# Performance work log

Measured on AMD Instinct MI355X. Metric: run time of the kernel, lower is better.

Reference implementation:

```python
import jax, jax.numpy as jnp
import numpy as np
import math

B, N, DMODEL, H = 8, 1024, 256, 8
HEAD_DIM = DMODEL // H


def setup_inputs() -> dict:
    key = jax.random.key(0)
    ks = jax.random.split(key, 8)
    x = jax.random.normal(ks[0], (B, N, DMODEL), dtype=jnp.float32)
    # symmetric-ish nonnegative pairwise distances
    adj = jax.random.uniform(ks[1], (B, N, N), dtype=jnp.float32) * 10.0
    mask = jax.random.uniform(ks[2], (B, N)) < 0.9  # bool, mostly valid nodes
    W_qkv = jax.random.normal(ks[3], (DMODEL, 3 * DMODEL), dtype=jnp.float32) / math.sqrt(DMODEL)
    b_qkv = jax.random.normal(ks[4], (3 * DMODEL,), dtype=jnp.float32) * 0.01
    shifts = jnp.arange(1.0, H + 1.0, dtype=jnp.float32)  # initial_shifts
    widths = jnp.ones((H,), dtype=jnp.float32)            # initial_widths
    # self_loop_W = 1/head_dim + U(0,1), non-trainable
    self_loop_w = 1.0 / HEAD_DIM + jax.random.uniform(ks[5], (H,), dtype=jnp.float32)
    return {"x": x, "adj": adj, "mask": mask, "W_qkv": W_qkv, "b_qkv": b_qkv,
            "shifts": shifts, "widths": widths, "self_loop_w": self_loop_w}


def reference(x, adj, mask, W_qkv, b_qkv, shifts, widths, self_loop_w):
    b, n, _ = x.shape
    h = shifts.shape[0]
    d = W_qkv.shape[1] // (3 * h)
    qkv = (x @ W_qkv + b_qkv).reshape(b, n, 3, h, d)
    qkv = jnp.transpose(qkv, (2, 0, 3, 1, 4))  # [3, B, H, N, D]
    Q, K, V = qkv[0], qkv[1], qkv[2]
    scores = jnp.einsum('bhnd,bhmd->bhnm', Q, K) / jnp.sqrt(jnp.float32(d))
    # Gaussian moire focus on adjacency distances, per head
    sh = shifts.reshape(1, h, 1, 1)
    w = jnp.maximum(widths, 0.5).reshape(1, h, 1, 1)
    moire = jnp.exp(-((adj[:, None, :, :] - sh) ** 2) / w)
    adjusted = scores + jnp.log(jnp.maximum(moire, 1e-6))
    eye = jnp.eye(n, dtype=adjusted.dtype)  # [N, N]
    adjusted = adjusted + eye * self_loop_w.reshape(1, h, 1, 1)
    mask2d = (mask[:, :, None] & mask[:, None, :])[:, None, :, :]  # [B,1,N,N]
    adjusted = jnp.where(mask2d, adjusted, jnp.float32(-1000000.0))
    attn = jax.nn.softmax(adjusted, axis=-1)
    out = jnp.einsum('bhnm,bhmd->bhnd', attn, V)
    return jnp.transpose(out, (0, 2, 1, 3)).reshape(b, n, h * d)
```

## Files before the change

### kernel.cpp

```cpp
#include <hip/hip_runtime.h>

#define BB 8
#define NN 1024
#define DM 256
#define HH 8
#define HD 32
#define TC 768

typedef __bf16 bf16x8 __attribute__((ext_vector_type(8)));
typedef __bf16 bf16x4 __attribute__((ext_vector_type(4)));
typedef float  f32x4  __attribute__((ext_vector_type(4)));
typedef int    i32x4  __attribute__((ext_vector_type(4)));
typedef unsigned int u32;

__global__ __launch_bounds__(256) void precast(
    const float* __restrict__ x, const float* __restrict__ W,
    __bf16* __restrict__ xb, __bf16* __restrict__ Wt)
{
  const int tid = threadIdx.x;
  const int bid = blockIdx.x;
  if (bid < 48) {
    __shared__ __bf16 T[64][65];
    const int ct = bid % 12, kt = bid / 12;
    const int c0 = ct * 64, k0 = kt * 64;
    #pragma unroll
    for (int i = 0; i < 16; ++i) {
      int e = tid + i * 256, kk = e >> 6, cc = e & 63;
      T[cc][kk] = (__bf16)W[(size_t)(k0 + kk) * TC + c0 + cc];
    }
    __syncthreads();
    #pragma unroll
    for (int i = 0; i < 16; ++i) {
      int e = tid + i * 256, cc = e >> 6, kk = e & 63;
      Wt[(size_t)(c0 + cc) * DM + k0 + kk] = T[cc][kk];
    }
  } else {
    const size_t e = (size_t)(bid - 48) * 256 + tid;
    const float4 v = ((const float4*)x)[e];
    bf16x4 o;
    o[0] = (__bf16)v.x; o[1] = (__bf16)v.y;
    o[2] = (__bf16)v.z; o[3] = (__bf16)v.w;
    ((bf16x4*)xb)[e] = o;
  }
}

__global__ __launch_bounds__(256, 3) void qkv_gemm(
    const __bf16* __restrict__ xb, const __bf16* __restrict__ Wt,
    const float* __restrict__ bias, __bf16* __restrict__ Qb,
    __bf16* __restrict__ Kb, __bf16* __restrict__ Vt)
{
  __shared__ __align__(16) char LDSU[49152];
  __bf16* As0 = (__bf16*)LDSU;
  __bf16* Bs0 = (__bf16*)(LDSU + 16384);
  __bf16* As1 = (__bf16*)(LDSU + 24576);
  __bf16* Bs1 = (__bf16*)(LDSU + 40960);

  const int tid  = threadIdx.x;
  const int w    = tid >> 6, lane = tid & 63;
  const int n16  = lane & 15, quad = lane >> 4;
  const int m0   = blockIdx.y * 128, c0 = blockIdx.x * 64;
  const int bb   = m0 >> 10, n0 = m0 & 1023;

  const int stRow = w*8 + (lane >> 3);
  const int stG   = (lane & 7) ^ (lane >> 3);
  const __bf16* gA = &xb[(size_t)(m0 + stRow)*DM + stG*8];
  const __bf16* gB = &Wt[(size_t)(c0 + stRow)*DM + stG*8];

#define QKV_STAGE(Adst, Bdst, K0) do {                                        \
    _Pragma("unroll")                                                         \
    for (int i_ = 0; i_ < 4; ++i_) {                                          \
      const __bf16* gp_ = gA + (size_t)(i_*32)*DM + (K0);                     \
      __bf16* lp_ = (Adst) + (i_*32 + w*8)*64;                                \
      __builtin_amdgcn_global_load_lds(                                       \
          (const __attribute__((address_space(1))) u32*)gp_,                  \
          (__attribute__((address_space(3))) u32*)lp_, 16, 0, 0);             \
    }                                                                         \
    _Pragma("unroll")                                                         \
    for (int i_ = 0; i_ < 2; ++i_) {                                          \
      const __bf16* gp_ = gB + (size_t)(i_*32)*DM + (K0);                     \
      __bf16* lp_ = (Bdst) + (i_*32 + w*8)*64;                                \
      __builtin_amdgcn_global_load_lds(                                       \
          (const __attribute__((address_space(1))) u32*)gp_,                  \
          (__attribute__((address_space(3))) u32*)lp_, 16, 0, 0);             \
    }                                                                         \
  } while (0)

  f32x4 acc[2][4] = {};

  QKV_STAGE(As0, Bs0, 0);
  __syncthreads();

  #pragma unroll
  for (int kk = 0; kk < 4; ++kk) {
    __bf16* Ac = (kk & 1) ? As1 : As0;
    __bf16* Bc = (kk & 1) ? Bs1 : Bs0;
    if (kk == 0)      QKV_STAGE(As1, Bs1, 64);
    else if (kk == 1) QKV_STAGE(As0, Bs0, 128);
    else if (kk == 2) QKV_STAGE(As1, Bs1, 192);
    #pragma unroll
    for (int ks = 0; ks < 2; ++ks) {
      const int ch = ((ks*4 + quad) ^ (n16 & 7)) * 8;
      bf16x8 af0 = *(const bf16x8*)&Ac[(w*32 + n16)*64 + ch];
      bf16x8 af1 = *(const bf16x8*)&Ac[(w*32 + 16 + n16)*64 + ch];
      #pragma unroll
      for (int cb = 0; cb < 4; ++cb) {
        bf16x8 bfb = *(const bf16x8*)&Bc[(cb*16 + n16)*64 + ch];
        acc[0][cb] = __builtin_amdgcn_mfma_f32_16x16x32_bf16(af0, bfb, acc[0][cb], 0, 0, 0);
        acc[1][cb] = __builtin_amdgcn_mfma_f32_16x16x32_bf16(af1, bfb, acc[1][cb], 0, 0, 0);
      }
    }
    __syncthreads();
  }

  float bv[4];
  #pragma unroll
  for (int cb = 0; cb < 4; ++cb) bv[cb] = bias[c0 + cb*16 + n16];

  if (c0 < 512) {
    __bf16* Ct = (__bf16*)LDSU;
    #pragma unroll
    for (int cb = 0; cb < 4; ++cb)
      #pragma unroll
      for (int mb = 0; mb < 2; ++mb)
        #pragma unroll
        for (int r = 0; r < 4; ++r)
          Ct[(w*32 + mb*16 + quad*4 + r)*72 + cb*16 + n16] =
              (__bf16)(acc[mb][cb][r] + bv[cb]);
    __syncthreads();
    const int chunk = tid & 3, hh = (tid >> 2) & 1, rbase = tid >> 3;
    const int c_head = c0 + hh*32;
    const int h = (c_head >> 5) & 7;
    __bf16* base = (c_head >> 8) ? Kb : Qb;
    #pragma unroll
    for (int it = 0; it < 4; ++it) {
      int rl = rbase + it*32;
      bf16x8 v = *(const bf16x8*)&Ct[rl*72 + hh*32 + chunk*8];
      *(bf16x8*)&base[((size_t)((bb*HH + h)*NN + n0 + rl))*HD + chunk*8] = v;
    }
  } else {
    __bf16* CtT = (__bf16*)LDSU;
    #pragma unroll
    for (int cb = 0; cb < 4; ++cb)
      #pragma unroll
      for (int mb = 0; mb < 2; ++mb) {
        bf16x4 t;
        #pragma unroll
        for (int r = 0; r < 4; ++r) t[r] = (__bf16)(acc[mb][cb][r] + bv[cb]);
        *(bf16x4*)&CtT[(cb*16 + n16)*136 + w*32 + mb*16 + quad*4] = t;
      }
    __syncthreads();
    const int col = tid >> 2, sg = tid & 3;
    const int c = c0 + col;
    const int h = (c >> 5) & 7, dd = c & 31;
    __bf16* dst = &Vt[((size_t)((bb*HH + h)*HD + dd))*NN + n0 + sg*32];
    const __bf16* srcp = &CtT[col*136 + sg*32];
    #pragma unroll
    for (int q2 = 0; q2 < 4; ++q2)
      *(bf16x8*)&dst[q2*8] = *(const bf16x8*)&srcp[q2*8];
  }
}

__global__ __launch_bounds__(256, 4) void attn_kernel(
    const __bf16* __restrict__ Q, const __bf16* __restrict__ K,
    const __bf16* __restrict__ Vt, const float* __restrict__ adj,
    const int* __restrict__ mask, const float* __restrict__ shifts,
    const float* __restrict__ widths, const float* __restrict__ slw,
    float* __restrict__ out)
{
  __shared__ __align__(16) __bf16 Ks[2][64][40];
  __shared__ __align__(16) __bf16 Vts[2][32][72];

  const int tid  = threadIdx.x;
  const int w    = tid >> 6, lane = tid & 63;
  const int n16  = lane & 15, quad = lane >> 4;
  const int bh   = blockIdx.x >> 4, qt = blockIdx.x & 15;
  const int b    = bh >> 3, h = bh & 7;
  const int q0   = qt * 64;

  const float L2E   = 1.4426950408889634f;
  const float sh    = shifts[h];
  const float ninvw = -L2E / fmaxf(widths[h], 0.5f);
  const float slv   = slw[h] * L2E;
  const float scl   = 0.17677669529663687f * L2E;
  const float MASKV = -28.0f;
  const float c1 = -2.0f * sh * ninvw;
  const float c2 = sh * sh * ninvw;

  const int srow = tid >> 2, sseg = tid & 3;
  const int phiRow = (srow & 35) + (((srow >> 2) & 1) << 4) + (((srow >> 3) & 3) << 2);
  const int vd   = tid >> 3, vsg  = tid & 7;

  const __bf16* Kg = K + (size_t)bh*NN*HD;
  const __bf16* Vg = Vt + (size_t)bh*HD*NN;

  const bf16x8 qf =
      *(const bf16x8*)&Q[((size_t)bh*NN + q0 + w*16 + n16)*HD + quad*8];

  {
    *(bf16x8*)&Ks[0][phiRow][sseg*8] = *(const bf16x8*)&Kg[srow*HD + sseg*8];
    *(bf16x8*)&Vts[0][vd][vsg*8]     = *(const bf16x8*)&Vg[(size_t)vd*NN + vsg*8];
  }

  const bool mqv = mask[b*NN + q0 + w*16 + n16] != 0;

  const float* aqp = adj + ((size_t)(b*NN + q0 + w*16 + n16))*NN + 8*quad;
  const int*   mjp = mask + b*NN + 8*quad;

  f32x4 av[2][2][2];
  #pragma unroll
  for (int a = 0; a < 2; ++a)
    #pragma unroll
    for (int b2 = 0; b2 < 2; ++b2)
      av[0][a][b2] = *(const f32x4*)&aqp[32*a + 4*b2];

  const int dloc8 = w*16 + n16 - 8*quad;

  const f32x4 zero = {0.f, 0.f, 0.f, 0.f};
  f32x4 o0 = zero, o1 = zero, lacc = zero;
  bf16x8 onesb;
  #pragma unroll
  for (int i = 0; i < 8; ++i) onesb[i] = (__bf16)1.0f;

  __syncthreads();

  #pragma unroll 2
  for (int jtl = 0; jtl < 16; ++jtl) {
    const int cur = jtl & 1, nxt = cur ^ 1;
    const int j0  = jtl * 64;

    bf16x8 kn, vn;
    if (jtl < 15) {
      kn = *(const bf16x8*)&Kg[(j0 + 64 + srow)*HD + sseg*8];
      vn = *(const bf16x8*)&Vg[(size_t)vd*NN + j0 + 64 + vsg*8];
      #pragma unroll
      for (int a = 0; a < 2; ++a)
        #pragma unroll
        for (int b2 = 0; b2 < 2; ++b2)
          av[nxt][a][b2] = *(const f32x4*)&aqp[j0 + 64 + 32*a + 4*b2];
    }

    i32x4 mj[2][2];
    #pragma unroll
    for (int a = 0; a < 2; ++a)
      #pragma unroll
      for (int b2 = 0; b2 < 2; ++b2)
        mj[a][b2] = *(const i32x4*)&mjp[j0 + 32*a + 4*b2];

    f32x4 s[4];
    #pragma unroll
    for (int c = 0; c < 4; ++c) {
      bf16x8 kf = *(const bf16x8*)&Ks[cur][c*16 + n16][quad*8];
      s[c] = __builtin_amdgcn_mfma_f32_16x16x32_bf16(kf, qf, zero, 0, 0, 0);
    }

    const bool diagtile = (jtl == qt);
    bf16x8 pa0, pa1;
    #pragma unroll
    for (int a = 0; a < 2; ++a)
      #pragma unroll
      for (int b2 = 0; b2 < 2; ++b2) {
        const int c = 2*a + b2;
        #pragma unroll
        for (int r = 0; r < 4; ++r) {
          float ad  = av[cur][a][b2][r];
          float mo  = fmaf(ad, fmaf(ad, ninvw, c1), c2);
          float val = fmaf(s[c][r], scl, mo);
          if (diagtile && (32*a + 4*b2 + r) == dloc8) val += slv;
          bool ok = mqv && (mj[a][b2][r] != 0);
          val = ok ? val : MASKV;
          float p = __builtin_amdgcn_exp2f(val);
          if (a == 0) pa0[4*b2 + r] = (__bf16)p;
          else        pa1[4*b2 + r] = (__bf16)p;
        }
      }

    bf16x8 b00 = *(const bf16x8*)&Vts[cur][n16][quad*8];
    bf16x8 b01 = *(const bf16x8*)&Vts[cur][n16][32 + quad*8];
    bf16x8 b10 = *(const bf16x8*)&Vts[cur][16 + n16][quad*8];
    bf16x8 b11 = *(const bf16x8*)&Vts[cur][16 + n16][32 + quad*8];
    o0   = __builtin_amdgcn_mfma_f32_16x16x32_bf16(pa0, b00, o0, 0, 0, 0);
    o0   = __builtin_amdgcn_mfma_f32_16x16x32_bf16(pa1, b01, o0, 0, 0, 0);
    o1   = __builtin_amdgcn_mfma_f32_16x16x32_bf16(pa0, b10, o1, 0, 0, 0);
    o1   = __builtin_amdgcn_mfma_f32_16x16x32_bf16(pa1, b11, o1, 0, 0, 0);
    lacc = __builtin_amdgcn_mfma_f32_16x16x32_bf16(pa0, onesb, lacc, 0, 0, 0);
    lacc = __builtin_amdgcn_mfma_f32_16x16x32_bf16(pa1, onesb, lacc, 0, 0, 0);

    if (jtl < 15) {
      *(bf16x8*)&Ks[nxt][phiRow][sseg*8] = kn;
      *(bf16x8*)&Vts[nxt][vd][vsg*8]     = vn;
    }
    __syncthreads();
  }

  #pragma unroll
  for (int r = 0; r < 4; ++r) {
    const float invl = 1.0f / lacc[r];
    const int n = q0 + w*16 + quad*4 + r;
    float* og = out + ((size_t)(b*NN + n))*DM + h*HD;
    og[n16]      = o0[r] * invl;
    og[16 + n16] = o1[r] * invl;
  }
}

extern "C" void kernel_launch(void* const* d_in, const int* in_sizes, int n_in,
                              void* d_out, int out_size, void* d_ws, size_t ws_size,
                              hipStream_t stream) {
  const float* x      = (const float*)d_in[0];
  const float* adj    = (const float*)d_in[1];
  const int*   mask   = (const int*)d_in[2];
  const float* W      = (const float*)d_in[3];
  const float* bias   = (const float*)d_in[4];
  const float* shifts = (const float*)d_in[5];
  const float* widths = (const float*)d_in[6];
  const float* slwp   = (const float*)d_in[7];
  float* out = (float*)d_out;

  const size_t BHND = (size_t)BB*HH*NN*HD;
  const size_t WTN  = (size_t)TC*DM;
  __bf16* xbuf = (__bf16*)d_ws;
  __bf16* Wt   = xbuf + BHND;
  __bf16* Qb   = Wt + WTN;
  __bf16* Kb   = Qb + BHND;
  __bf16* Vt   = Kb + BHND;

  precast<<<dim3(48 + (int)(BHND/4/256)), 256, 0, stream>>>(x, W, xbuf, Wt);
  qkv_gemm<<<dim3(TC/64, (BB*NN)/128), 256, 0, stream>>>(xbuf, Wt, bias, Qb, Kb, Vt);
  attn_kernel<<<dim3(BB*HH*16), 256, 0, stream>>>(Qb, Kb, Vt, adj, mask,
                                                  shifts, widths, slwp, out);
}
```

Baseline: 147.9 us.

## Remap key-to-lane layout and interleave exp computation with PV MFMAs

Changes which key columns each lane owns. K rows are now stored unpermuted, and V^T is permuted in LDS with split bf16x4 loads, so each lane reads adj and mask as four contiguous 16-column chunks instead of the earlier 32/4 interleave. The probability computation is split into two halves, and the first half's PV and row-sum MFMAs are issued before the second half's exp work, so matrix and vector work can overlap. The V loads become two narrower 8-byte global accesses per thread, which may cost some global-load efficiency.

```diff
diff --git a/kernel.cpp b/kernel.cpp
--- a/kernel.cpp
+++ b/kernel.cpp
@@ -187,8 +187,9 @@
   const float c2 = sh * sh * ninvw;
 
   const int srow = tid >> 2, sseg = tid & 3;
-  const int phiRow = (srow & 35) + (((srow >> 2) & 1) << 4) + (((srow >> 3) & 3) << 2);
   const int vd   = tid >> 3, vsg  = tid & 7;
+  const int vA   = (vsg & 4) << 3;
+  const int vq   = vsg & 3;
 
   const __bf16* Kg = K + (size_t)bh*NN*HD;
   const __bf16* Vg = Vt + (size_t)bh*HD*NN;
@@ -197,23 +198,21 @@
       *(const bf16x8*)&Q[((size_t)bh*NN + q0 + w*16 + n16)*HD + quad*8];
 
   {
-    *(bf16x8*)&Ks[0][phiRow][sseg*8] = *(const bf16x8*)&Kg[srow*HD + sseg*8];
-    *(bf16x8*)&Vts[0][vd][vsg*8]     = *(const bf16x8*)&Vg[(size_t)vd*NN + vsg*8];
+    *(bf16x8*)&Ks[0][srow][sseg*8] = *(const bf16x8*)&Kg[srow*HD + sseg*8];
+    *(bf16x4*)&Vts[0][vd][vsg*8]     = *(const bf16x4*)&Vg[(size_t)vd*NN + vA + 4*vq];
+    *(bf16x4*)&Vts[0][vd][vsg*8 + 4] = *(const bf16x4*)&Vg[(size_t)vd*NN + vA + 16 + 4*vq];
   }
 
   const bool mqv = mask[b*NN + q0 + w*16 + n16] != 0;
 
-  const float* aqp = adj + ((size_t)(b*NN + q0 + w*16 + n16))*NN + 8*quad;
-  const int*   mjp = mask + b*NN + 8*quad;
-
-  f32x4 av[2][2][2];
-  #pragma unroll
-  for (int a = 0; a < 2; ++a)
-    #pragma unroll
-    for (int b2 = 0; b2 < 2; ++b2)
-      av[0][a][b2] = *(const f32x4*)&aqp[32*a + 4*b2];
-
-  const int dloc8 = w*16 + n16 - 8*quad;
+  const float* aqp = adj + ((size_t)(b*NN + q0 + w*16 + n16))*NN + 4*quad;
+  const int*   mjp = mask + b*NN + 4*quad;
+
+  f32x4 av[2][4];
+  #pragma unroll
+  for (int c = 0; c < 4; ++c) av[0][c] = *(const f32x4*)&aqp[16*c];
+
+  const int dloc = w*16 + n16 - 4*quad;
 
   const f32x4 zero = {0.f, 0.f, 0.f, 0.f};
   f32x4 o0 = zero, o1 = zero, lacc = zero;
@@ -228,23 +227,19 @@
     const int cur = jtl & 1, nxt = cur ^ 1;
     const int j0  = jtl * 64;
 
-    bf16x8 kn, vn;
+    bf16x8 kn; bf16x4 vn0, vn1;
     if (jtl < 15) {
-      kn = *(const bf16x8*)&Kg[(j0 + 64 + srow)*HD + sseg*8];
-      vn = *(const bf16x8*)&Vg[(size_t)vd*NN + j0 + 64 + vsg*8];
-      #pragma unroll
-      for (int a = 0; a < 2; ++a)
-        #pragma unroll
-        for (int b2 = 0; b2 < 2; ++b2)
-          av[nxt][a][b2] = *(const f32x4*)&aqp[j0 + 64 + 32*a + 4*b2];
-    }
-
-    i32x4 mj[2][2];
-    #pragma unroll
-    for (int a = 0; a < 2; ++a)
-      #pragma unroll
-      for (int b2 = 0; b2 < 2; ++b2)
-        mj[a][b2] = *(const i32x4*)&mjp[j0 + 32*a + 4*b2];
+      kn  = *(const bf16x8*)&Kg[(j0 + 64 + srow)*HD + sseg*8];
+      vn0 = *(const bf16x4*)&Vg[(size_t)vd*NN + j0 + 64 + vA + 4*vq];
+      vn1 = *(const bf16x4*)&Vg[(size_t)vd*NN + j0 + 64 + vA + 16 + 4*vq];
+      #pragma unroll
+      for (int c = 0; c < 4; ++c)
+        av[nxt][c] = *(const f32x4*)&aqp[j0 + 64 + 16*c];
+    }
+
+    i32x4 mj[4];
+    #pragma unroll
+    for (int c = 0; c < 4; ++c) mj[c] = *(const i32x4*)&mjp[j0 + 16*c];
 
     f32x4 s[4];
     #pragma unroll
@@ -252,42 +247,49 @@
       bf16x8 kf = *(const bf16x8*)&Ks[cur][c*16 + n16][quad*8];
       s[c] = __builtin_amdgcn_mfma_f32_16x16x32_bf16(kf, qf, zero, 0, 0, 0);
     }
-
-    const bool diagtile = (jtl == qt);
-    bf16x8 pa0, pa1;
-    #pragma unroll
-    for (int a = 0; a < 2; ++a)
-      #pragma unroll
-      for (int b2 = 0; b2 < 2; ++b2) {
-        const int c = 2*a + b2;
-        #pragma unroll
-        for (int r = 0; r < 4; ++r) {
-          float ad  = av[cur][a][b2][r];
-          float mo  = fmaf(ad, fmaf(ad, ninvw, c1), c2);
-          float val = fmaf(s[c][r], scl, mo);
-          if (diagtile && (32*a + 4*b2 + r) == dloc8) val += slv;
-          bool ok = mqv && (mj[a][b2][r] != 0);
-          val = ok ? val : MASKV;
-          float p = __builtin_amdgcn_exp2f(val);
-          if (a == 0) pa0[4*b2 + r] = (__bf16)p;
-          else        pa1[4*b2 + r] = (__bf16)p;
-        }
-      }
 
     bf16x8 b00 = *(const bf16x8*)&Vts[cur][n16][quad*8];
     bf16x8 b01 = *(const bf16x8*)&Vts[cur][n16][32 + quad*8];
     bf16x8 b10 = *(const bf16x8*)&Vts[cur][16 + n16][quad*8];
     bf16x8 b11 = *(const bf16x8*)&Vts[cur][16 + n16][32 + quad*8];
+
+    const bool diagtile = (jtl == qt);
+    bf16x8 pa0, pa1;
+    #pragma unroll
+    for (int c = 0; c < 2; ++c)
+      #pragma unroll
+      for (int r = 0; r < 4; ++r) {
+        float ad  = av[cur][c][r];
+        float mo  = fmaf(ad, fmaf(ad, ninvw, c1), c2);
+        float val = fmaf(s[c][r], scl, mo);
+        if (diagtile && (16*c + r == dloc)) val += slv;
+        bool ok = mqv && (mj[c][r] != 0);
+        val = ok ? val : MASKV;
+        pa0[c*4 + r] = (__bf16)__builtin_amdgcn_exp2f(val);
+      }
     o0   = __builtin_amdgcn_mfma_f32_16x16x32_bf16(pa0, b00, o0, 0, 0, 0);
+    o1   = __builtin_amdgcn_mfma_f32_16x16x32_bf16(pa0, b10, o1, 0, 0, 0);
+    lacc = __builtin_amdgcn_mfma_f32_16x16x32_bf16(pa0, onesb, lacc, 0, 0, 0);
+    #pragma unroll
+    for (int c = 2; c < 4; ++c)
+      #pragma unroll
+      for (int r = 0; r < 4; ++r) {
+        float ad  = av[cur][c][r];
+        float mo  = fmaf(ad, fmaf(ad, ninvw, c1), c2);
+        float val = fmaf(s[c][r], scl, mo);
+        if (diagtile && (16*c + r == dloc)) val += slv;
+        bool ok = mqv && (mj[c][r] != 0);
+        val = ok ? val : MASKV;
+        pa1[(c & 1)*4 + r] = (__bf16)__builtin_amdgcn_exp2f(val);
+      }
     o0   = __builtin_amdgcn_mfma_f32_16x16x32_bf16(pa1, b01, o0, 0, 0, 0);
-    o1   = __builtin_amdgcn_mfma_f32_16x16x32_bf16(pa0, b10, o1, 0, 0, 0);
     o1   = __builtin_amdgcn_mfma_f32_16x16x32_bf16(pa1, b11, o1, 0, 0, 0);
-    lacc = __builtin_amdgcn_mfma_f32_16x16x32_bf16(pa0, onesb, lacc, 0, 0, 0);
     lacc = __builtin_amdgcn_mfma_f32_16x16x32_bf16(pa1, onesb, lacc, 0, 0, 0);
 
     if (jtl < 15) {
-      *(bf16x8*)&Ks[nxt][phiRow][sseg*8] = kn;
-      *(bf16x8*)&Vts[nxt][vd][vsg*8]     = vn;
+      *(bf16x8*)&Ks[nxt][srow][sseg*8]     = kn;
+      *(bf16x4*)&Vts[nxt][vd][vsg*8]       = vn0;
+      *(bf16x4*)&Vts[nxt][vd][vsg*8 + 4]   = vn1;
     }
     __syncthreads();
   }
```

Measured after the change: 151.3 us. +2.3%, slower.

## Share adjacency tiles across heads by assigning one head per wave

Applied to the files above, without the earlier changes.

The attention kernel now gives each block 32 query rows and 4 heads, one head per wave. The fp32 adjacency tile is staged once in shared memory and read by all four heads, so each adj row is fetched from global memory twice rather than eight times. Each wave handles its own K/V tile in private LDS buffers and routes P through LDS to reach the MFMA A-layout. The cost is more LDS traffic and bank pressure, fewer blocks (512), lower occupancy (launch bounds 2), and a block-wide barrier each tile.

```diff
diff --git a/kernel.cpp b/kernel.cpp
--- a/kernel.cpp
+++ b/kernel.cpp
@@ -10,7 +10,6 @@
 typedef __bf16 bf16x8 __attribute__((ext_vector_type(8)));
 typedef __bf16 bf16x4 __attribute__((ext_vector_type(4)));
 typedef float  f32x4  __attribute__((ext_vector_type(4)));
-typedef int    i32x4  __attribute__((ext_vector_type(4)));
 typedef unsigned int u32;
 
 __global__ __launch_bounds__(256) void precast(
@@ -160,22 +159,27 @@
   }
 }
 
-__global__ __launch_bounds__(256, 4) void attn_kernel(
+__global__ __launch_bounds__(256, 2) void attn_kernel(
     const __bf16* __restrict__ Q, const __bf16* __restrict__ K,
     const __bf16* __restrict__ Vt, const float* __restrict__ adj,
     const int* __restrict__ mask, const float* __restrict__ shifts,
     const float* __restrict__ widths, const float* __restrict__ slw,
     float* __restrict__ out)
 {
-  __shared__ __align__(16) __bf16 Ks[2][64][40];
-  __shared__ __align__(16) __bf16 Vts[2][32][72];
+  __shared__ __align__(16) __bf16 Ks[4][64][40];
+  __shared__ __align__(16) __bf16 Vts[4][32][72];
+  __shared__ __align__(16) float  As[2][32][68];
+  __shared__ __align__(16) __bf16 Ps[4][16][72];
 
   const int tid  = threadIdx.x;
   const int w    = tid >> 6, lane = tid & 63;
   const int n16  = lane & 15, quad = lane >> 4;
-  const int bh   = blockIdx.x >> 4, qt = blockIdx.x & 15;
-  const int b    = bh >> 3, h = bh & 7;
-  const int q0   = qt * 64;
+  const int hg   = blockIdx.x & 1;
+  const int qt   = (blockIdx.x >> 1) & 31;
+  const int b    = blockIdx.x >> 6;
+  const int h    = hg*4 + w;
+  const int bh   = b*HH + h;
+  const int q0   = qt * 32;
 
   const float L2E   = 1.4426950408889634f;
   const float sh    = shifts[h];
@@ -186,120 +190,133 @@
   const float c1 = -2.0f * sh * ninvw;
   const float c2 = sh * sh * ninvw;
 
-  const int srow = tid >> 2, sseg = tid & 3;
-  const int phiRow = (srow & 35) + (((srow >> 2) & 1) << 4) + (((srow >> 3) & 3) << 2);
-  const int vd   = tid >> 3, vsg  = tid & 7;
-
   const __bf16* Kg = K + (size_t)bh*NN*HD;
   const __bf16* Vg = Vt + (size_t)bh*HD*NN;
 
-  const bf16x8 qf =
-      *(const bf16x8*)&Q[((size_t)bh*NN + q0 + w*16 + n16)*HD + quad*8];
+  const __bf16* kgp = Kg + (size_t)lane*HD;
+  const int vdr = lane >> 1, vc0 = (lane & 1)*32;
+  const __bf16* vgp = Vg + (size_t)vdr*NN + vc0;
+  const int arow = tid >> 3, ac = (tid & 7)*4;
+  const float* agp = adj + ((size_t)(b*NN + q0 + arow))*NN + ac;
+  const int* mjp = mask + b*NN + n16;
+
+  const bf16x8 qf0 = *(const bf16x8*)&Q[((size_t)bh*NN + q0 +      n16)*HD + quad*8];
+  const bf16x8 qf1 = *(const bf16x8*)&Q[((size_t)bh*NN + q0 + 16 + n16)*HD + quad*8];
+  int mq[2][4];
+  #pragma unroll
+  for (int g = 0; g < 2; ++g)
+    #pragma unroll
+    for (int r = 0; r < 4; ++r)
+      mq[g][r] = mask[b*NN + q0 + g*16 + quad*4 + r];
 
   {
-    *(bf16x8*)&Ks[0][phiRow][sseg*8] = *(const bf16x8*)&Kg[srow*HD + sseg*8];
-    *(bf16x8*)&Vts[0][vd][vsg*8]     = *(const bf16x8*)&Vg[(size_t)vd*NN + vsg*8];
-  }
-
-  const bool mqv = mask[b*NN + q0 + w*16 + n16] != 0;
-
-  const float* aqp = adj + ((size_t)(b*NN + q0 + w*16 + n16))*NN + 8*quad;
-  const int*   mjp = mask + b*NN + 8*quad;
-
-  f32x4 av[2][2][2];
-  #pragma unroll
-  for (int a = 0; a < 2; ++a)
-    #pragma unroll
-    for (int b2 = 0; b2 < 2; ++b2)
-      av[0][a][b2] = *(const f32x4*)&aqp[32*a + 4*b2];
-
-  const int dloc8 = w*16 + n16 - 8*quad;
+    bf16x8 k0[4], v0[4]; f32x4 aa, ab;
+    #pragma unroll
+    for (int c = 0; c < 4; ++c) k0[c] = *(const bf16x8*)&kgp[c*8];
+    #pragma unroll
+    for (int i = 0; i < 4; ++i) v0[i] = *(const bf16x8*)&vgp[i*8];
+    aa = *(const f32x4*)&agp[0]; ab = *(const f32x4*)&agp[32];
+    #pragma unroll
+    for (int c = 0; c < 4; ++c) *(bf16x8*)&Ks[w][lane][c*8] = k0[c];
+    #pragma unroll
+    for (int i = 0; i < 4; ++i) *(bf16x8*)&Vts[w][vdr][vc0 + i*8] = v0[i];
+    *(f32x4*)&As[0][arow][ac]      = aa;
+    *(f32x4*)&As[0][arow][32 + ac] = ab;
+  }
+  int mj[4];
+  #pragma unroll
+  for (int cb = 0; cb < 4; ++cb) mj[cb] = mjp[cb*16];
 
   const f32x4 zero = {0.f, 0.f, 0.f, 0.f};
-  f32x4 o0 = zero, o1 = zero, lacc = zero;
+  f32x4 o0[2] = {zero, zero}, o1[2] = {zero, zero}, lacc[2] = {zero, zero};
   bf16x8 onesb;
   #pragma unroll
   for (int i = 0; i < 8; ++i) onesb[i] = (__bf16)1.0f;
 
+  const int diagT = qt >> 1;
+  const int dbase = (qt & 1) * 32;
+
   __syncthreads();
 
-  #pragma unroll 2
   for (int jtl = 0; jtl < 16; ++jtl) {
-    const int cur = jtl & 1, nxt = cur ^ 1;
+    const int cur = jtl & 1;
     const int j0  = jtl * 64;
 
-    bf16x8 kn, vn;
+    bf16x8 kn[4], vn[4]; f32x4 an0, an1; int mjn[4];
     if (jtl < 15) {
-      kn = *(const bf16x8*)&Kg[(j0 + 64 + srow)*HD + sseg*8];
-      vn = *(const bf16x8*)&Vg[(size_t)vd*NN + j0 + 64 + vsg*8];
-      #pragma unroll
-      for (int a = 0; a < 2; ++a)
+      #pragma unroll
+      for (int c = 0; c < 4; ++c) kn[c] = *(const bf16x8*)&kgp[(size_t)(j0+64)*HD + c*8];
+      #pragma unroll
+      for (int i = 0; i < 4; ++i) vn[i] = *(const bf16x8*)&vgp[j0 + 64 + i*8];
+      an0 = *(const f32x4*)&agp[j0 + 64];
+      an1 = *(const f32x4*)&agp[j0 + 96];
+      #pragma unroll
+      for (int cb = 0; cb < 4; ++cb) mjn[cb] = mjp[j0 + 64 + cb*16];
+    }
+
+    bf16x8 b00 = *(const bf16x8*)&Vts[w][n16][quad*8];
+    bf16x8 b01 = *(const bf16x8*)&Vts[w][n16][32 + quad*8];
+    bf16x8 b10 = *(const bf16x8*)&Vts[w][16 + n16][quad*8];
+    bf16x8 b11 = *(const bf16x8*)&Vts[w][16 + n16][32 + quad*8];
+
+    const bool diagtile = (jtl == diagT);
+
+    #pragma unroll
+    for (int g = 0; g < 2; ++g) {
+      const bf16x8 qf = g ? qf1 : qf0;
+      f32x4 s[4];
+      #pragma unroll
+      for (int cb = 0; cb < 4; ++cb) {
+        bf16x8 kf = *(const bf16x8*)&Ks[w][cb*16 + n16][quad*8];
+        s[cb] = __builtin_amdgcn_mfma_f32_16x16x32_bf16(qf, kf, zero, 0, 0, 0);
+      }
+      const int dref = dbase + g*16 + quad*4;
+      #pragma unroll
+      for (int r = 0; r < 4; ++r) {
         #pragma unroll
-        for (int b2 = 0; b2 < 2; ++b2)
-          av[nxt][a][b2] = *(const f32x4*)&aqp[j0 + 64 + 32*a + 4*b2];
-    }
-
-    i32x4 mj[2][2];
-    #pragma unroll
-    for (int a = 0; a < 2; ++a)
-      #pragma unroll
-      for (int b2 = 0; b2 < 2; ++b2)
-        mj[a][b2] = *(const i32x4*)&mjp[j0 + 32*a + 4*b2];
-
-    f32x4 s[4];
-    #pragma unroll
-    for (int c = 0; c < 4; ++c) {
-      bf16x8 kf = *(const bf16x8*)&Ks[cur][c*16 + n16][quad*8];
-      s[c] = __builtin_amdgcn_mfma_f32_16x16x32_bf16(kf, qf, zero, 0, 0, 0);
-    }
-
-    const bool diagtile = (jtl == qt);
-    bf16x8 pa0, pa1;
-    #pragma unroll
-    for (int a = 0; a < 2; ++a)
-      #pragma unroll
-      for (int b2 = 0; b2 < 2; ++b2) {
-        const int c = 2*a + b2;
-        #pragma unroll
-        for (int r = 0; r < 4; ++r) {
-          float ad  = av[cur][a][b2][r];
-          float mo  = fmaf(ad, fmaf(ad, ninvw, c1), c2);
-          float val = fmaf(s[c][r], scl, mo);
-          if (diagtile && (32*a + 4*b2 + r) == dloc8) val += slv;
-          bool ok = mqv && (mj[a][b2][r] != 0);
+        for (int cb = 0; cb < 4; ++cb) {
+          float a   = As[cur][g*16 + quad*4 + r][cb*16 + n16];
+          float mo  = fmaf(a, fmaf(a, ninvw, c1), c2);
+          float val = fmaf(s[cb][r], scl, mo);
+          if (diagtile && (cb*16 + n16 == dref + r)) val += slv;
+          bool ok = (mq[g][r] != 0) && (mj[cb] != 0);
           val = ok ? val : MASKV;
-          float p = __builtin_amdgcn_exp2f(val);
-          if (a == 0) pa0[4*b2 + r] = (__bf16)p;
-          else        pa1[4*b2 + r] = (__bf16)p;
+          Ps[w][quad*4 + r][cb*16 + n16] = (__bf16)__builtin_amdgcn_exp2f(val);
         }
       }
-
-    bf16x8 b00 = *(const bf16x8*)&Vts[cur][n16][quad*8];
-    bf16x8 b01 = *(const bf16x8*)&Vts[cur][n16][32 + quad*8];
-    bf16x8 b10 = *(const bf16x8*)&Vts[cur][16 + n16][quad*8];
-    bf16x8 b11 = *(const bf16x8*)&Vts[cur][16 + n16][32 + quad*8];
-    o0   = __builtin_amdgcn_mfma_f32_16x16x32_bf16(pa0, b00, o0, 0, 0, 0);
-    o0   = __builtin_amdgcn_mfma_f32_16x16x32_bf16(pa1, b01, o0, 0, 0, 0);
-    o1   = __builtin_amdgcn_mfma_f32_16x16x32_bf16(pa0, b10, o1, 0, 0, 0);
-    o1   = __builtin_amdgcn_mfma_f32_16x16x32_bf16(pa1, b11, o1, 0, 0, 0);
-    lacc = __builtin_amdgcn_mfma_f32_16x16x32_bf16(pa0, onesb, lacc, 0, 0, 0);
-    lacc = __builtin_amdgcn_mfma_f32_16x16x32_bf16(pa1, onesb, lacc, 0, 0, 0);
+      bf16x8 a0 = *(const bf16x8*)&Ps[w][n16][quad*8];
+      bf16x8 a1 = *(const bf16x8*)&Ps[w][n16][32 + quad*8];
+      o0[g]   = __builtin_amdgcn_mfma_f32_16x16x32_bf16(a0, b00, o0[g], 0, 0, 0);
+      o0[g]   = __builtin_amdgcn_mfma_f32_16x16x32_bf16(a1, b01, o0[g], 0, 0, 0);
+      o1[g]   = __builtin_amdgcn_mfma_f32_16x16x32_bf16(a0, b10, o1[g], 0, 0, 0);
+      o1[g]   = __builtin_amdgcn_mfma_f32_16x16x32_bf16(a1, b11, o1[g], 0, 0, 0);
+      lacc[g] = __builtin_amdgcn_mfma_f32_16x16x32_bf16(a0, onesb, lacc[g], 0, 0, 0);
+      lacc[g] = __builtin_amdgcn_mfma_f32_16x16x32_bf16(a1, onesb, lacc[g], 0, 0, 0);
+    }
 
     if (jtl < 15) {
-      *(bf16x8*)&Ks[nxt][phiRow][sseg*8] = kn;
-      *(bf16x8*)&Vts[nxt][vd][vsg*8]     = vn;
-    }
-    __syncthreads();
-  }
-
-  #pragma unroll
-  for (int r = 0; r < 4; ++r) {
-    const float invl = 1.0f / lacc[r];
-    const int n = q0 + w*16 + quad*4 + r;
-    float* og = out + ((size_t)(b*NN + n))*DM + h*HD;
-    og[n16]      = o0[r] * invl;
-    og[16 + n16] = o1[r] * invl;
-  }
+      #pragma unroll
+      for (int c = 0; c < 4; ++c) *(bf16x8*)&Ks[w][lane][c*8] = kn[c];
+      #pragma unroll
+      for (int i = 0; i < 4; ++i) *(bf16x8*)&Vts[w][vdr][vc0 + i*8] = vn[i];
+      *(f32x4*)&As[1 - cur][arow][ac]      = an0;
+      *(f32x4*)&As[1 - cur][arow][32 + ac] = an1;
+      #pragma unroll
+      for (int cb = 0; cb < 4; ++cb) mj[cb] = mjn[cb];
+    }
+    __syncthreads();
+  }
+
+  #pragma unroll
+  for (int g = 0; g < 2; ++g)
+    #pragma unroll
+    for (int r = 0; r < 4; ++r) {
+      const float invl = 1.0f / lacc[g][r];
+      const int n = q0 + g*16 + quad*4 + r;
+      float* og = out + ((size_t)(b*NN + n))*DM + h*HD;
+      og[n16]      = o0[g][r] * invl;
+      og[16 + n16] = o1[g][r] * invl;
+    }
 }
 
 extern "C" void kernel_launch(void* const* d_in, const int* in_sizes, int n_in,
@@ -325,6 +342,6 @@
 
   precast<<<dim3(48 + (int)(BHND/4/256)), 256, 0, stream>>>(x, W, xbuf, Wt);
   qkv_gemm<<<dim3(TC/64, (BB*NN)/128), 256, 0, stream>>>(xbuf, Wt, bias, Qb, Kb, Vt);
-  attn_kernel<<<dim3(BB*HH*16), 256, 0, stream>>>(Qb, Kb, Vt, adj, mask,
-                                                  shifts, widths, slwp, out);
+  attn_kernel<<<dim3(BB*32*2), 256, 0, stream>>>(Qb, Kb, Vt, adj, mask,
+                                                 shifts, widths, slwp, out);
 }
```

Measured after the change: 140.4 us. 1.05x faster.
